# Optimization experiments

Measured on AMD Instinct MI355X. Metric: run time of the kernel, lower is better.

Reference implementation:

```python
import jax, jax.numpy as jnp
import numpy as np

N = 50000       # num_nodes
R = 32          # num_relations
H = 16          # hidden channels
C = 8           # num_classes
E = 1_600_000   # num_edges (avg degree 32)


def setup_inputs() -> dict:
    key = jax.random.key(0)
    ks = jax.random.split(key, 8)
    edge_index = jax.random.randint(ks[0], (2, E), 0, N, dtype=jnp.int64)
    edge_type = jnp.sort(jax.random.randint(ks[1], (E,), 0, R, dtype=jnp.int64))
    s1 = 1.0 / np.sqrt(N)
    s2 = 1.0 / np.sqrt(H)
    return {
        "edge_index": edge_index,
        "edge_type": edge_type,
        "weight1": jax.random.normal(ks[2], (R, N, H), jnp.float32) * s1,
        "root1": jax.random.normal(ks[3], (N, H), jnp.float32) * s1,
        "bias1": jnp.zeros((H,), jnp.float32),
        "weight2": jax.random.normal(ks[4], (R, H, C), jnp.float32) * s2,
        "root2": jax.random.normal(ks[5], (H, C), jnp.float32) * s2,
        "bias2": jnp.zeros((C,), jnp.float32),
    }


def reference(edge_index, edge_type, weight1, root1, bias1, weight2, root2, bias2):
    # R-GCN with mean aggregation per relation (PyG RGCNConv semantics).
    src, dst = edge_index[0], edge_index[1]
    # combined segment id: one segment per (relation, dst node)
    seg = edge_type * N + dst  # [E]
    ones = jnp.ones((E,), weight1.dtype)
    cnt = jax.ops.segment_sum(ones, seg, num_segments=R * N)          # [R*N]
    denom = jnp.maximum(cnt, 1.0)[:, None]

    # ---- layer 1: x = None -> identity features; message_r(j) = weight1[r, j] ----
    msg1 = weight1[edge_type, src]                                     # [E, H] gather
    mean1 = jax.ops.segment_sum(msg1, seg, num_segments=R * N) / denom # [R*N, H]
    h = mean1.reshape(R, N, H).sum(0) + root1 + bias1                  # [N, H]
    h = jax.nn.relu(h)

    # ---- layer 2: aggregate features per relation, then relation-specific GEMM ----
    msg2 = h[src]                                                       # [E, H]
    mean2 = jax.ops.segment_sum(msg2, seg, num_segments=R * N) / denom  # [R*N, H]
    mean2 = mean2.reshape(R, N, H)
    out = jnp.einsum('rnf,rfo->no', mean2, weight2) + h @ root2 + bias2 # [N, C]
    return jax.nn.log_softmax(out, axis=1)
```

## Files before the change

### kernel.cpp

```cpp
#include <hip/hip_runtime.h>
#include <math.h>

#define NN 50000
#define RR 32
#define HH 16
#define CC 8
#define SHIFT 6
#define BSZ 64
#define NB 782
#define G 128
#define BINS (BSZ * RR)
#define STAGE_MAX 4096
#define SCH 64

static __device__ __forceinline__ unsigned short f2bf(float x) {
    unsigned u = __float_as_uint(x);
    unsigned r = (u + 0x7FFF + ((u >> 16) & 1)) >> 16;
    return (unsigned short)r;
}


__global__ void hist_k(const int* __restrict__ dst, int* __restrict__ hist, int E) {
    __shared__ int lh[NB];
    int g = blockIdx.x, tid = threadIdx.x;
    for (int j = tid; j < NB; j += 256) lh[j] = 0;
    __syncthreads();
    int chunk = (E + G - 1) / G;
    int beg = g * chunk, end = min(beg + chunk, E);
    for (int i = beg + tid; i < end; i += 256)
        atomicAdd(&lh[dst[i] >> SHIFT], 1);
    __syncthreads();
    for (int j = tid; j < NB; j += 256) hist[g * NB + j] = lh[j];
}

__global__ void scanA_k(const int* __restrict__ hist, int* __restrict__ btot) {
    __shared__ int red[2];
    int b = blockIdx.x, t = threadIdx.x;
    int v = hist[t * NB + b];
#pragma unroll
    for (int m = 1; m < 64; m <<= 1) v += __shfl_xor(v, m);
    if ((t & 63) == 0) red[t >> 6] = v;
    __syncthreads();
    if (t == 0) btot[b] = red[0] + red[1];
}

__global__ void scanB_k(const int* __restrict__ btot, int* __restrict__ boff) {
    __shared__ int lds[1024];
    int t = threadIdx.x;
    int v = (t < NB) ? btot[t] : 0;
    lds[t] = v;
    __syncthreads();
    for (int ofs = 1; ofs < 1024; ofs <<= 1) {
        int add = (t >= ofs) ? lds[t - ofs] : 0;
        __syncthreads();
        lds[t] += add;
        __syncthreads();
    }
    if (t < NB) boff[t] = lds[t] - v;
    if (t == NB - 1) boff[NB] = lds[t];
}

__global__ void scanC_k(const int* __restrict__ hist, const int* __restrict__ boff,
                        int* __restrict__ pos) {
    __shared__ int lds[G];
    int b = blockIdx.x, t = threadIdx.x;
    int v = hist[t * NB + b];
    lds[t] = v;
    __syncthreads();
    for (int ofs = 1; ofs < G; ofs <<= 1) {
        int add = (t >= ofs) ? lds[t - ofs] : 0;
        __syncthreads();
        lds[t] += add;
        __syncthreads();
    }
    pos[t * NB + b] = boff[b] + lds[t] - v;
}

__global__ void scatter2_k(const int* __restrict__ src, const int* __restrict__ dst,
                           const int* __restrict__ et, const int* __restrict__ pos,
                           unsigned* __restrict__ bucket, int E) {
    __shared__ int cur[NB];
    int g = blockIdx.x, tid = threadIdx.x;
    for (int j = tid; j < NB; j += 256) cur[j] = pos[g * NB + j];
    __syncthreads();
    int chunk = (E + G - 1) / G;
    int beg = g * chunk, end = min(beg + chunk, E);
    for (int i = beg + tid; i < end; i += 256) {
        int d = dst[i];
        int p = atomicAdd(&cur[d >> SHIFT], 1);
        bucket[p] = (unsigned)src[i] | ((unsigned)et[i] << 16) |
                    ((unsigned)(d & (BSZ - 1)) << 21);
    }
}


__global__ __launch_bounds__(256) void sortfin_k(
        const unsigned* __restrict__ bucket, const int* __restrict__ boff,
        unsigned* __restrict__ sorted, int* __restrict__ off, float* __restrict__ inv) {
    __shared__ int bins[BINS];
    __shared__ unsigned stage[STAGE_MAX];
    __shared__ int ts[256];
    int b = blockIdx.x, t = threadIdx.x;
    int e0 = boff[b], n = boff[b + 1] - e0;
    int d0 = b * BSZ;
    int ndst = NN - d0; if (ndst > BSZ) ndst = BSZ;
    for (int j = t; j < BINS; j += 256) bins[j] = 0;
    __syncthreads();
    for (int i = t; i < n; i += 256) {
        unsigned rec = bucket[e0 + i];
        int key = ((rec >> 21) & 63) * RR + ((rec >> 16) & 31);
        atomicAdd(&bins[key], 1);
    }
    __syncthreads();
    for (int j = t; j < ndst * RR; j += 256)
        inv[d0 * RR + j] = 1.0f / fmaxf((float)bins[j], 1.0f);
    int loc[8]; int s = 0;
#pragma unroll
    for (int k = 0; k < 8; ++k) { loc[k] = bins[t * 8 + k]; s += loc[k]; }
    ts[t] = s;
    __syncthreads();
    for (int ofs = 1; ofs < 256; ofs <<= 1) {
        int add = (t >= ofs) ? ts[t - ofs] : 0;
        __syncthreads();
        ts[t] += add;
        __syncthreads();
    }
    int run = ts[t] - s;
    __syncthreads();
#pragma unroll
    for (int k = 0; k < 8; ++k) { int c = loc[k]; bins[t * 8 + k] = run; run += c; }
    __syncthreads();
    for (int dl = t; dl < ndst; dl += 256) off[d0 + dl] = e0 + bins[dl * RR];
    if (b == NB - 1 && t == 0) off[NN] = e0 + n;
    __syncthreads();
    if (n <= STAGE_MAX) {
        for (int i = t; i < n; i += 256) {
            unsigned rec = bucket[e0 + i];
            int key = ((rec >> 21) & 63) * RR + ((rec >> 16) & 31);
            int p = atomicAdd(&bins[key], 1);
            stage[p] = rec & 0x1FFFFF;
        }
        __syncthreads();
        for (int i = t; i < n; i += 256) sorted[e0 + i] = stage[i];
    } else {
        for (int i = t; i < n; i += 256) {
            unsigned rec = bucket[e0 + i];
            int key = ((rec >> 21) & 63) * RR + ((rec >> 16) & 31);
            int p = atomicAdd(&bins[key], 1);
            sorted[e0 + p] = rec & 0x1FFFFF;
        }
    }
}


__global__ __launch_bounds__(256) void layer1_k(
        const unsigned* __restrict__ sorted, const int* __restrict__ off,
        const float* __restrict__ inv, const float4* __restrict__ w1v,
        const float4* __restrict__ root1v, const float4* __restrict__ bias1v,
        float4* __restrict__ hv) {
    int d = (blockIdx.x * blockDim.x + threadIdx.x) >> 6;
    if (d >= NN) return;
    int lane = threadIdx.x & 63;
    int q = lane & 3;
    int b0 = off[d], b1 = off[d + 1];
    float4 acc = make_float4(0.f, 0.f, 0.f, 0.f);
    for (int i = b0 + (lane >> 2); i < b1; i += 16) {
        unsigned rec = sorted[i];
        int s = rec & 0xFFFF, r = (rec >> 16) & 31;
        float sc = inv[d * RR + r];
        float4 w = w1v[(size_t)(r * NN + s) * 4 + q];
        acc.x += w.x * sc; acc.y += w.y * sc; acc.z += w.z * sc; acc.w += w.w * sc;
    }
#pragma unroll
    for (int m = 4; m < 64; m <<= 1) {
        acc.x += __shfl_xor(acc.x, m); acc.y += __shfl_xor(acc.y, m);
        acc.z += __shfl_xor(acc.z, m); acc.w += __shfl_xor(acc.w, m);
    }
    if (lane < 4) {
        float4 rt = root1v[d * 4 + lane];
        float4 bs = bias1v[lane];
        float4 o;
        o.x = fmaxf(acc.x + rt.x + bs.x, 0.f);
        o.y = fmaxf(acc.y + rt.y + bs.y, 0.f);
        o.z = fmaxf(acc.z + rt.z + bs.z, 0.f);
        o.w = fmaxf(acc.w + rt.w + bs.w, 0.f);
        hv[d * 4 + lane] = o;
    }
}


__global__ __launch_bounds__(256) void hwbuild_k(
        const float* __restrict__ h, const float* __restrict__ w2,
        unsigned* __restrict__ hw2) {
    __shared__ float4 hs[SCH * 4];
    int tid = threadIdx.x;
    int r = tid >> 3, c = tid & 7;
    float4 w0, w1, w2r, w3;
    {
        const float* wb = w2 + (r * HH) * CC + c;
        w0 = make_float4(wb[0*CC], wb[1*CC], wb[2*CC], wb[3*CC]);
        w1 = make_float4(wb[4*CC], wb[5*CC], wb[6*CC], wb[7*CC]);
        w2r = make_float4(wb[8*CC], wb[9*CC], wb[10*CC], wb[11*CC]);
        w3 = make_float4(wb[12*CC], wb[13*CC], wb[14*CC], wb[15*CC]);
    }
    int s0 = blockIdx.x * SCH;
    int nnodes = NN - s0; if (nnodes > SCH) nnodes = SCH;
    const float4* hg = (const float4*)(h + s0 * HH);
    for (int j = tid; j < nnodes * 4; j += 256) hs[j] = hg[j];
    __syncthreads();
    for (int sl = 0; sl < nnodes; ++sl) {
        float4 h0 = hs[sl * 4 + 0], h1 = hs[sl * 4 + 1];
        float4 h2 = hs[sl * 4 + 2], h3 = hs[sl * 4 + 3];
        float acc = h0.x * w0.x + h0.y * w0.y + h0.z * w0.z + h0.w * w0.w
                  + h1.x * w1.x + h1.y * w1.y + h1.z * w1.z + h1.w * w1.w
                  + h2.x * w2r.x + h2.y * w2r.y + h2.z * w2r.z + h2.w * w2r.w
                  + h3.x * w3.x + h3.y * w3.y + h3.z * w3.z + h3.w * w3.w;
        float other = __shfl_xor(acc, 1);
        if ((c & 1) == 0) {
            unsigned packed = (unsigned)f2bf(acc) | ((unsigned)f2bf(other) << 16);
            hw2[((size_t)(s0 + sl) * (RR * CC) + tid) >> 1] = packed;
        }
    }
}


__global__ __launch_bounds__(256) void layer2_k(
        const unsigned* __restrict__ sorted, const int* __restrict__ off,
        const float* __restrict__ inv, const unsigned short* __restrict__ hw2,
        const float* __restrict__ h, const float* __restrict__ root2,
        const float* __restrict__ bias2, float* __restrict__ out) {
    int d = (blockIdx.x * blockDim.x + threadIdx.x) >> 6;
    if (d >= NN) return;
    int lane = threadIdx.x & 63;
    int sub = lane >> 3, c = lane & 7;
    int b0 = off[d], b1 = off[d + 1];
    float acc = 0.f;
    for (int i = b0 + sub; i < b1; i += 8) {
        unsigned rec = sorted[i];
        int s = rec & 0xFFFF, r = (rec >> 16) & 31;
        unsigned short us = hw2[(size_t)s * (RR * CC) + r * CC + c];
        float val = __uint_as_float((unsigned)us << 16);
        acc += val * inv[d * RR + r];
    }
    acc += __shfl_xor(acc, 8);
    acc += __shfl_xor(acc, 16);
    acc += __shfl_xor(acc, 32);
    if (lane < 8) {
        float v = acc + bias2[c];
        const float* hd = h + d * HH;
#pragma unroll
        for (int f = 0; f < HH; ++f) v += hd[f] * root2[f * CC + c];
        float m = v;
        m = fmaxf(m, __shfl_xor(m, 1));
        m = fmaxf(m, __shfl_xor(m, 2));
        m = fmaxf(m, __shfl_xor(m, 4));
        float ex = expf(v - m);
        float ssum = ex;
        ssum += __shfl_xor(ssum, 1);
        ssum += __shfl_xor(ssum, 2);
        ssum += __shfl_xor(ssum, 4);
        out[d * CC + c] = v - m - logf(ssum);
    }
}


extern "C" void kernel_launch(void* const* d_in, const int* in_sizes, int n_in,
                              void* d_out, int out_size, void* d_ws, size_t ws_size,
                              hipStream_t stream) {
    const int*   edge_index = (const int*)d_in[0];
    const int*   edge_type  = (const int*)d_in[1];
    const float* weight1    = (const float*)d_in[2];
    const float* root1      = (const float*)d_in[3];
    const float* bias1      = (const float*)d_in[4];
    const float* weight2    = (const float*)d_in[5];
    const float* root2      = (const float*)d_in[6];
    const float* bias2      = (const float*)d_in[7];
    float* out = (float*)d_out;

    const int E = in_sizes[1];
    const int* src = edge_index;
    const int* dst = edge_index + E;

    char* base = (char*)d_ws;
    size_t hw2_bytes = sizeof(unsigned short) * (size_t)NN * RR * CC;
    unsigned* hw2 = (unsigned*)base;

    char* p = base;
    auto suballoc = [&](size_t bytes) -> void* {
        void* r = (void*)p; p += (bytes + 255) & ~(size_t)255; return r;
    };
    int*      hist   = (int*)     suballoc(sizeof(int) * (size_t)G * NB);
    int*      pos    = (int*)     suballoc(sizeof(int) * (size_t)G * NB);
    unsigned* bucket = (unsigned*)suballoc(sizeof(unsigned) * (size_t)E);

    p = base + ((hw2_bytes + 255) & ~(size_t)255);
    int*      btot   = (int*)     suballoc(sizeof(int) * NB);
    int*      boff   = (int*)     suballoc(sizeof(int) * (NB + 1));
    int*      off    = (int*)     suballoc(sizeof(int) * (NN + 1));
    unsigned* sorted = (unsigned*)suballoc(sizeof(unsigned) * (size_t)E);
    float*    inv    = (float*)   suballoc(sizeof(float) * (size_t)NN * RR);
    float*    h      = (float*)   suballoc(sizeof(float) * (size_t)NN * HH);
    (void)ws_size;

    hist_k<<<G, 256, 0, stream>>>(dst, hist, E);
    scanA_k<<<NB, G, 0, stream>>>(hist, btot);
    scanB_k<<<1, 1024, 0, stream>>>(btot, boff);
    scanC_k<<<NB, G, 0, stream>>>(hist, boff, pos);
    scatter2_k<<<G, 256, 0, stream>>>(src, dst, edge_type, pos, bucket, E);
    sortfin_k<<<NB, 256, 0, stream>>>(bucket, boff, sorted, off, inv);

    int nblk = (NN * 64 + 255) / 256;
    layer1_k<<<nblk, 256, 0, stream>>>(sorted, off, inv, (const float4*)weight1,
                                       (const float4*)root1, (const float4*)bias1,
                                       (float4*)h);
    hwbuild_k<<<(NN + SCH - 1) / SCH, 256, 0, stream>>>(h, weight2, hw2);
    layer2_k<<<nblk, 256, 0, stream>>>(sorted, off, inv,
                                       (const unsigned short*)hw2, h,
                                       root2, bias2, out);
}
```

Before: 162.4 us.

## Double histogram groups, use nontemporal weight loads, restructure hw2 build

```diff
diff --git a/kernel.cpp b/kernel.cpp
--- a/kernel.cpp
+++ b/kernel.cpp
@@ -8,10 +8,12 @@
 #define SHIFT 6
 #define BSZ 64
 #define NB 782
-#define G 128
+#define G 256
 #define BINS (BSZ * RR)
 #define STAGE_MAX 4096
 #define SCH 64
+
+typedef float floatx4 __attribute__((ext_vector_type(4)));
 
 static __device__ __forceinline__ unsigned short f2bf(float x) {
     unsigned u = __float_as_uint(x);
@@ -34,14 +36,14 @@
 }
 
 __global__ void scanA_k(const int* __restrict__ hist, int* __restrict__ btot) {
-    __shared__ int red[2];
+    __shared__ int red[4];
     int b = blockIdx.x, t = threadIdx.x;
     int v = hist[t * NB + b];
 #pragma unroll
     for (int m = 1; m < 64; m <<= 1) v += __shfl_xor(v, m);
     if ((t & 63) == 0) red[t >> 6] = v;
     __syncthreads();
-    if (t == 0) btot[b] = red[0] + red[1];
+    if (t == 0) btot[b] = red[0] + red[1] + red[2] + red[3];
 }
 
 __global__ void scanB_k(const int* __restrict__ btot, int* __restrict__ boff) {
@@ -155,7 +157,7 @@
 
 __global__ __launch_bounds__(256) void layer1_k(
         const unsigned* __restrict__ sorted, const int* __restrict__ off,
-        const float* __restrict__ inv, const float4* __restrict__ w1v,
+        const float* __restrict__ inv, const floatx4* __restrict__ w1v,
         const float4* __restrict__ root1v, const float4* __restrict__ bias1v,
         float4* __restrict__ hv) {
     int d = (blockIdx.x * blockDim.x + threadIdx.x) >> 6;
@@ -163,27 +165,27 @@
     int lane = threadIdx.x & 63;
     int q = lane & 3;
     int b0 = off[d], b1 = off[d + 1];
-    float4 acc = make_float4(0.f, 0.f, 0.f, 0.f);
+    float ax = 0.f, ay = 0.f, az = 0.f, aw = 0.f;
     for (int i = b0 + (lane >> 2); i < b1; i += 16) {
         unsigned rec = sorted[i];
         int s = rec & 0xFFFF, r = (rec >> 16) & 31;
         float sc = inv[d * RR + r];
-        float4 w = w1v[(size_t)(r * NN + s) * 4 + q];
-        acc.x += w.x * sc; acc.y += w.y * sc; acc.z += w.z * sc; acc.w += w.w * sc;
+        floatx4 w = __builtin_nontemporal_load(&w1v[(size_t)(r * NN + s) * 4 + q]);
+        ax += w.x * sc; ay += w.y * sc; az += w.z * sc; aw += w.w * sc;
     }
 #pragma unroll
     for (int m = 4; m < 64; m <<= 1) {
-        acc.x += __shfl_xor(acc.x, m); acc.y += __shfl_xor(acc.y, m);
-        acc.z += __shfl_xor(acc.z, m); acc.w += __shfl_xor(acc.w, m);
+        ax += __shfl_xor(ax, m); ay += __shfl_xor(ay, m);
+        az += __shfl_xor(az, m); aw += __shfl_xor(aw, m);
     }
     if (lane < 4) {
         float4 rt = root1v[d * 4 + lane];
         float4 bs = bias1v[lane];
         float4 o;
-        o.x = fmaxf(acc.x + rt.x + bs.x, 0.f);
-        o.y = fmaxf(acc.y + rt.y + bs.y, 0.f);
-        o.z = fmaxf(acc.z + rt.z + bs.z, 0.f);
-        o.w = fmaxf(acc.w + rt.w + bs.w, 0.f);
+        o.x = fmaxf(ax + rt.x + bs.x, 0.f);
+        o.y = fmaxf(ay + rt.y + bs.y, 0.f);
+        o.z = fmaxf(az + rt.z + bs.z, 0.f);
+        o.w = fmaxf(aw + rt.w + bs.w, 0.f);
         hv[d * 4 + lane] = o;
     }
 }
@@ -191,35 +193,37 @@
 
 __global__ __launch_bounds__(256) void hwbuild_k(
         const float* __restrict__ h, const float* __restrict__ w2,
-        unsigned* __restrict__ hw2) {
+        unsigned* __restrict__ hw2u) {
     __shared__ float4 hs[SCH * 4];
     int tid = threadIdx.x;
-    int r = tid >> 3, c = tid & 7;
-    float4 w0, w1, w2r, w3;
+    int nl = tid >> 7;
+    int k  = tid & 127;
+    int r  = k >> 2;
+    int c0 = (k & 3) * 2;
+    float wa[HH], wb[HH];
     {
-        const float* wb = w2 + (r * HH) * CC + c;
-        w0 = make_float4(wb[0*CC], wb[1*CC], wb[2*CC], wb[3*CC]);
-        w1 = make_float4(wb[4*CC], wb[5*CC], wb[6*CC], wb[7*CC]);
-        w2r = make_float4(wb[8*CC], wb[9*CC], wb[10*CC], wb[11*CC]);
-        w3 = make_float4(wb[12*CC], wb[13*CC], wb[14*CC], wb[15*CC]);
+        const float* base = w2 + r * HH * CC;
+#pragma unroll
+        for (int f = 0; f < HH; ++f) {
+            wa[f] = base[f * CC + c0];
+            wb[f] = base[f * CC + c0 + 1];
+        }
     }
     int s0 = blockIdx.x * SCH;
     int nnodes = NN - s0; if (nnodes > SCH) nnodes = SCH;
     const float4* hg = (const float4*)(h + s0 * HH);
     for (int j = tid; j < nnodes * 4; j += 256) hs[j] = hg[j];
     __syncthreads();
-    for (int sl = 0; sl < nnodes; ++sl) {
+    for (int sl = nl; sl < nnodes; sl += 2) {
         float4 h0 = hs[sl * 4 + 0], h1 = hs[sl * 4 + 1];
         float4 h2 = hs[sl * 4 + 2], h3 = hs[sl * 4 + 3];
-        float acc = h0.x * w0.x + h0.y * w0.y + h0.z * w0.z + h0.w * w0.w
-                  + h1.x * w1.x + h1.y * w1.y + h1.z * w1.z + h1.w * w1.w
-                  + h2.x * w2r.x + h2.y * w2r.y + h2.z * w2r.z + h2.w * w2r.w
-                  + h3.x * w3.x + h3.y * w3.y + h3.z * w3.z + h3.w * w3.w;
-        float other = __shfl_xor(acc, 1);
-        if ((c & 1) == 0) {
-            unsigned packed = (unsigned)f2bf(acc) | ((unsigned)f2bf(other) << 16);
-            hw2[((size_t)(s0 + sl) * (RR * CC) + tid) >> 1] = packed;
-        }
+        float hr[HH] = {h0.x, h0.y, h0.z, h0.w, h1.x, h1.y, h1.z, h1.w,
+                        h2.x, h2.y, h2.z, h2.w, h3.x, h3.y, h3.z, h3.w};
+        float va = 0.f, vb = 0.f;
+#pragma unroll
+        for (int f = 0; f < HH; ++f) { va += hr[f] * wa[f]; vb += hr[f] * wb[f]; }
+        unsigned packed = (unsigned)f2bf(va) | ((unsigned)f2bf(vb) << 16);
+        hw2u[(size_t)(s0 + sl) * 128 + k] = packed;
     }
 }
 
@@ -303,14 +307,14 @@
     (void)ws_size;
 
     hist_k<<<G, 256, 0, stream>>>(dst, hist, E);
-    scanA_k<<<NB, G, 0, stream>>>(hist, btot);
+    scanA_k<<<NB, 256, 0, stream>>>(hist, btot);
     scanB_k<<<1, 1024, 0, stream>>>(btot, boff);
     scanC_k<<<NB, G, 0, stream>>>(hist, boff, pos);
     scatter2_k<<<G, 256, 0, stream>>>(src, dst, edge_type, pos, bucket, E);
     sortfin_k<<<NB, 256, 0, stream>>>(bucket, boff, sorted, off, inv);
 
     int nblk = (NN * 64 + 255) / 256;
-    layer1_k<<<nblk, 256, 0, stream>>>(sorted, off, inv, (const float4*)weight1,
+    layer1_k<<<nblk, 256, 0, stream>>>(sorted, off, inv, (const floatx4*)weight1,
                                        (const float4*)root1, (const float4*)bias1,
                                        (float4*)h);
     hwbuild_k<<<(NN + SCH - 1) / SCH, 256, 0, stream>>>(h, weight2, hw2);
```

After: 159.1 us. -2.1%, faster.
